# Kernel tuning notes

Hardware: AMD Instinct MI355X
Metric: run time of the kernel (lower is better)

The kernel has to match this reference:

```python
import jax, jax.numpy as jnp
import numpy as np

B, L, HIDDEN, DEPTH, INPUT_DIM = 256, 4096, 128, 2, 2
LOG_PROB_FACTOR = 0.5


def setup_inputs() -> dict:
    key = jax.random.key(0)
    k1, k2, k3, k4 = jax.random.split(key, 4)
    x = jax.random.randint(k1, (B, L), 0, INPUT_DIM)
    # variance-scaling-like init (fan_avg), small scale for recurrent stability
    W_in = jax.random.normal(k2, (INPUT_DIM, HIDDEN), dtype=jnp.float32) * np.float32(
        (2.0 / (INPUT_DIM + HIDDEN)) ** 0.5)
    W_c = jax.random.normal(k3, (DEPTH, HIDDEN, HIDDEN), dtype=jnp.float32) * np.float32(
        (0.1 / HIDDEN) ** 0.5)
    W_out = jax.random.normal(k4, (HIDDEN, INPUT_DIM - 1), dtype=jnp.float32) * np.float32(
        (2.0 / (HIDDEN + INPUT_DIM - 1)) ** 0.5)
    b_out = jnp.zeros((INPUT_DIM - 1,), dtype=jnp.float32)
    return {"x": x, "W_in": W_in, "W_c": W_c, "W_out": W_out, "b_out": b_out}


def reference(x, W_in, W_c, W_out, b_out):
    # x: [B, L] int spins; returns per-sample summed log-prob [B]
    b, l = x.shape
    input_dim = W_in.shape[0]
    depth, hidden = W_c.shape[0], W_c.shape[1]

    oh = jax.nn.one_hot(x, input_dim, dtype=W_in.dtype)       # [B, L, D_in]
    xs = jnp.moveaxis(oh, 1, 0)                                # [L, B, D_in]

    h0 = jnp.zeros((b, depth, hidden), dtype=W_in.dtype)       # zero_carry
    prev0 = jnp.zeros((b, input_dim), dtype=W_in.dtype)        # initial input

    def step(carry, x_t):
        h, prev = carry
        # data_in_dense + actFun (shared across the stack call)
        r = jax.nn.elu(prev @ W_in)                            # [B, H]
        new_h = []
        for j in range(depth):
            # RNNCell: elu(cell_carry_dense(h_j)) + input
            hj = jax.nn.elu(h[:, j] @ W_c[j]) + r              # [B, H]
            new_h.append(hj)
            r = hj
        h_new = jnp.stack(new_h, axis=1)                       # [B, depth, H]
        # output head -> normalized log-probs (realValuedOutput=True)
        logits = r @ W_out + b_out                             # [B, D_in-1]
        amp = jnp.concatenate(
            [jnp.zeros((b, 1), dtype=logits.dtype), logits], axis=-1)  # [B, D_in]
        lp = LOG_PROB_FACTOR * jax.nn.log_softmax(amp, axis=-1)
        log_p = jnp.sum(lp * x_t, axis=-1)                     # [B]
        log_p = jnp.nan_to_num(log_p, nan=-35.0)
        return (h_new, x_t), log_p

    _, log_ps = jax.lax.scan(step, (h0, prev0), xs)            # [L, B]
    return jnp.sum(log_ps, axis=0)                             # [B]
```

## Files before the change

### kernel.cpp

```cpp
#include <hip/hip_runtime.h>
#include <hip/hip_bf16.h>


#define L_LEN 4096
#define HID   128
#define NB    16
#define TPB   256
#define WPITCH 129

typedef float f32x4 __attribute__((ext_vector_type(4)));
typedef short s16x8 __attribute__((ext_vector_type(8)));
typedef short s16x4 __attribute__((ext_vector_type(4)));

__device__ __forceinline__ float eluf(float v) { return v > 0.f ? v : (__expf(v) - 1.f); }
__device__ __forceinline__ unsigned short f2bf(float v) {
    union { __hip_bfloat16 b; unsigned short u; } cv;
    cv.b = __float2bfloat16(v);
    return cv.u;
}

__global__ __launch_bounds__(TPB, 1)
void rnn_swap_kernel(const int*   __restrict__ x,
                     const float* __restrict__ W_in,
                     const float* __restrict__ W_c,
                     const float* __restrict__ W_out,
                     const float* __restrict__ b_out,
                     float* __restrict__ out)
{
    __shared__ __align__(16) unsigned short hAf[2][2][NB][HID];
    __shared__ unsigned xbsm[NB * WPITCH];
    __shared__ float gbuf[2][4][NB];

    const int T = threadIdx.x;
    const int w = T >> 6, l = T & 63, c = l & 15, g = l >> 4;
    const int bb0 = blockIdx.x * NB;
    const int swz = (c & 7) << 3;

    for (int idx = w; idx < NB * (L_LEN / 64); idx += 4) {
        int batch = idx >> 6;
        int pos   = ((idx & 63) << 6) + l;
        int v     = x[(bb0 + batch) * L_LEN + pos];
        unsigned long long mask = __ballot(v & 1);
        if (l == 0)  xbsm[batch * WPITCH + ((idx & 63) << 1)]     = (unsigned)mask;
        if (l == 32) xbsm[batch * WPITCH + ((idx & 63) << 1) + 1] = (unsigned)(mask >> 32);
    }
    for (int i = T; i < 2 * 2 * NB * HID; i += TPB) ((unsigned short*)hAf)[i] = 0;

    s16x8 Af[2][2][4];
    #pragma unroll
    for (int layer = 0; layer < 2; ++layer)
      #pragma unroll
      for (int mt = 0; mt < 2; ++mt) {
        const int col = w * 32 + mt * 16 + c;
        #pragma unroll
        for (int kt = 0; kt < 4; ++kt) {
            s16x8 f;
            #pragma unroll
            for (int j = 0; j < 8; ++j)
                f[j] = (short)f2bf(W_c[(layer * HID + kt * 32 + g * 8 + j) * HID + col]);
            Af[layer][mt][kt] = f;
        }
      }
    s16x8 woA;
    #pragma unroll
    for (int j = 0; j < 8; ++j)
        woA[j] = (c == 0) ? (short)f2bf(W_out[w * 32 + g * 8 + j]) : (short)0;

    float R0v[2][4], R1v[2][4];
    #pragma unroll
    for (int mt = 0; mt < 2; ++mt)
      #pragma unroll
      for (int r = 0; r < 4; ++r) {
        int co = w * 32 + mt * 16 + 4 * g + r;
        R0v[mt][r] = eluf(W_in[co]);
        R1v[mt][r] = eluf(W_in[HID + co]);
      }
    const float b0 = b_out[0];

    const int ro0 = (0 * 32 + g * 8) ^ swz, ro1 = (1 * 32 + g * 8) ^ swz;
    const int ro2 = (2 * 32 + g * 8) ^ swz, ro3 = (3 * 32 + g * 8) ^ swz;
    const int wo0 = (w * 32 + 0 * 16 + 4 * g) ^ swz;
    const int wo1 = (w * 32 + 1 * 16 + 4 * g) ^ swz;

    float acc = 0.f;
    unsigned xw = 0;

    __syncthreads();

#define STEP(T_, Q_) do {                                                     \
    const int t_ = (T_);                                                      \
    s16x8 B1v[4], B0v[4];                                                     \
    B1v[0] = *(const s16x8*)&hAf[Q_][1][c][ro0];                              \
    B1v[1] = *(const s16x8*)&hAf[Q_][1][c][ro1];                              \
    B1v[2] = *(const s16x8*)&hAf[Q_][1][c][ro2];                              \
    B1v[3] = *(const s16x8*)&hAf[Q_][1][c][ro3];                              \
    if (t_ < L_LEN) {                                                         \
        B0v[0] = *(const s16x8*)&hAf[Q_][0][c][ro0];                          \
        B0v[1] = *(const s16x8*)&hAf[Q_][0][c][ro1];                          \
        B0v[2] = *(const s16x8*)&hAf[Q_][0][c][ro2];                          \
        B0v[3] = *(const s16x8*)&hAf[Q_][0][c][ro3];                          \
        if (((t_ - 1) & 31) == 0) xw = xbsm[c * WPITCH + ((t_ - 1) >> 5)];    \
    }                                                                         \
    {                               \
        s16x8 Bw = (w == 0) ? B1v[0] : (w == 1) ? B1v[1]                      \
                 : (w == 2) ? B1v[2] : B1v[3];                                \
        f32x4 Cg = {0.f, 0.f, 0.f, 0.f};                                      \
        Cg = __builtin_amdgcn_mfma_f32_16x16x32_bf16(woA, Bw, Cg, 0, 0, 0);   \
        if (g == 0) gbuf[Q_][w][c] = Cg[0];                                   \
    }                                                                         \
    if (t_ > 1 && T < NB) {                         \
        int s = t_ - 2;                                                       \
        float gg = gbuf[Q_ ^ 1][0][T] + gbuf[Q_ ^ 1][1][T]                    \
                 + gbuf[Q_ ^ 1][2][T] + gbuf[Q_ ^ 1][3][T] + b0;              \
        unsigned cw = xbsm[T * WPITCH + (s >> 5)];                            \
        int bit = (cw >> (s & 31)) & 1;                                       \
        float mm  = fmaxf(gg, 0.f);                                           \
        float lse = mm + __logf(__expf(gg - mm) + __expf(-mm));               \
        acc += 0.5f * ((bit ? gg : 0.f) - lse);                               \
    }                                                                         \
    if (t_ < L_LEN) {                                                         \
        f32x4 C0v[2], C1v[2];                                                 \
        _Pragma("unroll")                                                     \
        for (int mt = 0; mt < 2; ++mt) {                                      \
            f32x4 c0 = {0.f, 0.f, 0.f, 0.f};                                  \
            f32x4 c1 = {0.f, 0.f, 0.f, 0.f};                                  \
            _Pragma("unroll")                                                 \
            for (int kt = 0; kt < 4; ++kt) {                                  \
                c0 = __builtin_amdgcn_mfma_f32_16x16x32_bf16(                 \
                        Af[0][mt][kt], B0v[kt], c0, 0, 0, 0);                 \
                c1 = __builtin_amdgcn_mfma_f32_16x16x32_bf16(                 \
                        Af[1][mt][kt], B1v[kt], c1, 0, 0, 0);                 \
            }                                                                 \
            C0v[mt] = c0; C1v[mt] = c1;                                       \
        }                                                                     \
        const int bit = (int)((xw >> ((t_ - 1) & 31)) & 1u);                  \
        _Pragma("unroll")                                                     \
        for (int mt = 0; mt < 2; ++mt) {                                      \
            s16x4 p0, p1;                                                     \
            _Pragma("unroll")                                                 \
            for (int r = 0; r < 4; ++r) {                                     \
                float h0 = eluf(C0v[mt][r]) + (bit ? R1v[mt][r] : R0v[mt][r]);\
                float h1 = eluf(C1v[mt][r]) + h0;                             \
                p0[r] = (short)f2bf(h0);                                      \
                p1[r] = (short)f2bf(h1);                                      \
            }                                                                 \
            const int wof = (mt == 0) ? wo0 : wo1;                            \
            *(s16x4*)&hAf[Q_ ^ 1][0][c][wof] = p0;                            \
            *(s16x4*)&hAf[Q_ ^ 1][1][c][wof] = p1;                            \
        }                                                                     \
    }                                                                         \
    __syncthreads();                                                          \
} while (0)

    for (int t = 1; t <= L_LEN; t += 2) {
        STEP(t, 1);
        STEP(t + 1, 0);
    }
#undef STEP

    if (T < NB) {
        float gg = gbuf[0][0][T] + gbuf[0][1][T] + gbuf[0][2][T] + gbuf[0][3][T] + b0;
        unsigned cw = xbsm[T * WPITCH + ((L_LEN - 1) >> 5)];
        int bit = (cw >> ((L_LEN - 1) & 31)) & 1;
        float mm  = fmaxf(gg, 0.f);
        float lse = mm + __logf(__expf(gg - mm) + __expf(-mm));
        acc += 0.5f * ((bit ? gg : 0.f) - lse);
        out[bb0 + T] = acc;
    }
}

extern "C" void kernel_launch(void* const* d_in, const int* in_sizes, int n_in,
                              void* d_out, int out_size, void* d_ws, size_t ws_size,
                              hipStream_t stream)
{
    const int*   x     = (const int*)  d_in[0];
    const float* W_in  = (const float*)d_in[1];
    const float* W_c   = (const float*)d_in[2];
    const float* W_out = (const float*)d_in[3];
    const float* b_out = (const float*)d_in[4];
    float* out = (float*)d_out;

    rnn_swap_kernel<<<16, TPB, 0, stream>>>(x, W_in, W_c, W_out, b_out, out);
}
```

Baseline: 3.129 ms.

## Pack two independent 16-batch groups per block with 512 threads

Each block now runs two independent 16-sample recurrences, one per 256-thread half. Shared hidden-state, gate and spin-bit buffers gain a group index, and the grid shrinks from 16 to 8 blocks. The goal is to interleave two independent dependency chains on the same compute unit to hide MFMA and LDS latency. The cost is double the work per SIMD at each step and a block-wide barrier across 8 waves instead of 4. The LDS swizzle also widens from (c&7)<<3 to c<<3, which changes the bank-conflict pattern.

```diff
diff --git a/kernel.cpp b/kernel.cpp
--- a/kernel.cpp
+++ b/kernel.cpp
@@ -4,8 +4,7 @@
 
 #define L_LEN 4096
 #define HID   128
-#define NB    16
-#define TPB   256
+#define TPB   512
 #define WPITCH 129
 
 typedef float f32x4 __attribute__((ext_vector_type(4)));
@@ -20,23 +19,27 @@
 }
 
 __global__ __launch_bounds__(TPB, 1)
-void rnn_swap_kernel(const int*   __restrict__ x,
-                     const float* __restrict__ W_in,
-                     const float* __restrict__ W_c,
-                     const float* __restrict__ W_out,
-                     const float* __restrict__ b_out,
-                     float* __restrict__ out)
+void rnn_g2_kernel(const int*   __restrict__ x,
+                   const float* __restrict__ W_in,
+                   const float* __restrict__ W_c,
+                   const float* __restrict__ W_out,
+                   const float* __restrict__ b_out,
+                   float* __restrict__ out)
 {
-    __shared__ __align__(16) unsigned short hAf[2][2][NB][HID];
-    __shared__ unsigned xbsm[NB * WPITCH];
-    __shared__ float gbuf[2][4][NB];
+    __shared__ __align__(16) unsigned short hAf[2][2][2][16][HID];
+    __shared__ unsigned xbsm[32 * WPITCH];
+    __shared__ float gbuf[2][2][4][16];
 
-    const int T = threadIdx.x;
-    const int w = T >> 6, l = T & 63, c = l & 15, g = l >> 4;
-    const int bb0 = blockIdx.x * NB;
-    const int swz = (c & 7) << 3;
+    const int T  = threadIdx.x;
+    const int w8 = T >> 6;
+    const int wg = T >> 8;
+    const int w  = w8 & 3;
+    const int l  = T & 63, c = l & 15, g = l >> 4;
+    const int grpT = T & 255;
+    const int bb0 = blockIdx.x * 32;
+    const int swz = c << 3;
 
-    for (int idx = w; idx < NB * (L_LEN / 64); idx += 4) {
+    for (int idx = w8; idx < 32 * (L_LEN / 64); idx += 8) {
         int batch = idx >> 6;
         int pos   = ((idx & 63) << 6) + l;
         int v     = x[(bb0 + batch) * L_LEN + pos];
@@ -44,7 +47,7 @@
         if (l == 0)  xbsm[batch * WPITCH + ((idx & 63) << 1)]     = (unsigned)mask;
         if (l == 32) xbsm[batch * WPITCH + ((idx & 63) << 1) + 1] = (unsigned)(mask >> 32);
     }
-    for (int i = T; i < 2 * 2 * NB * HID; i += TPB) ((unsigned short*)hAf)[i] = 0;
+    for (int i = T; i < 2 * 2 * 2 * 16 * HID; i += TPB) ((unsigned short*)hAf)[i] = 0;
 
     s16x8 Af[2][2][4];
     #pragma unroll
@@ -90,29 +93,30 @@
 #define STEP(T_, Q_) do {                                                     \
     const int t_ = (T_);                                                      \
     s16x8 B1v[4], B0v[4];                                                     \
-    B1v[0] = *(const s16x8*)&hAf[Q_][1][c][ro0];                              \
-    B1v[1] = *(const s16x8*)&hAf[Q_][1][c][ro1];                              \
-    B1v[2] = *(const s16x8*)&hAf[Q_][1][c][ro2];                              \
-    B1v[3] = *(const s16x8*)&hAf[Q_][1][c][ro3];                              \
+    B1v[0] = *(const s16x8*)&hAf[wg][Q_][1][c][ro0];                          \
+    B1v[1] = *(const s16x8*)&hAf[wg][Q_][1][c][ro1];                          \
+    B1v[2] = *(const s16x8*)&hAf[wg][Q_][1][c][ro2];                          \
+    B1v[3] = *(const s16x8*)&hAf[wg][Q_][1][c][ro3];                          \
     if (t_ < L_LEN) {                                                         \
-        B0v[0] = *(const s16x8*)&hAf[Q_][0][c][ro0];                          \
-        B0v[1] = *(const s16x8*)&hAf[Q_][0][c][ro1];                          \
-        B0v[2] = *(const s16x8*)&hAf[Q_][0][c][ro2];                          \
-        B0v[3] = *(const s16x8*)&hAf[Q_][0][c][ro3];                          \
-        if (((t_ - 1) & 31) == 0) xw = xbsm[c * WPITCH + ((t_ - 1) >> 5)];    \
+        B0v[0] = *(const s16x8*)&hAf[wg][Q_][0][c][ro0];                      \
+        B0v[1] = *(const s16x8*)&hAf[wg][Q_][0][c][ro1];                      \
+        B0v[2] = *(const s16x8*)&hAf[wg][Q_][0][c][ro2];                      \
+        B0v[3] = *(const s16x8*)&hAf[wg][Q_][0][c][ro3];                      \
+        if (((t_ - 1) & 31) == 0)                                             \
+            xw = xbsm[(wg * 16 + c) * WPITCH + ((t_ - 1) >> 5)];              \
     }                                                                         \
     {                               \
         s16x8 Bw = (w == 0) ? B1v[0] : (w == 1) ? B1v[1]                      \
                  : (w == 2) ? B1v[2] : B1v[3];                                \
         f32x4 Cg = {0.f, 0.f, 0.f, 0.f};                                      \
         Cg = __builtin_amdgcn_mfma_f32_16x16x32_bf16(woA, Bw, Cg, 0, 0, 0);   \
-        if (g == 0) gbuf[Q_][w][c] = Cg[0];                                   \
+        if (g == 0) gbuf[Q_][wg][w][c] = Cg[0];                               \
     }                                                                         \
-    if (t_ > 1 && T < NB) {                         \
+    if (t_ > 1 && grpT < 16) {                      \
         int s = t_ - 2;                                                       \
-        float gg = gbuf[Q_ ^ 1][0][T] + gbuf[Q_ ^ 1][1][T]                    \
-                 + gbuf[Q_ ^ 1][2][T] + gbuf[Q_ ^ 1][3][T] + b0;              \
-        unsigned cw = xbsm[T * WPITCH + (s >> 5)];                            \
+        float gg = gbuf[Q_ ^ 1][wg][0][grpT] + gbuf[Q_ ^ 1][wg][1][grpT]      \
+                 + gbuf[Q_ ^ 1][wg][2][grpT] + gbuf[Q_ ^ 1][wg][3][grpT] + b0;\
+        unsigned cw = xbsm[(wg * 16 + grpT) * WPITCH + (s >> 5)];             \
         int bit = (cw >> (s & 31)) & 1;                                       \
         float mm  = fmaxf(gg, 0.f);                                           \
         float lse = mm + __logf(__expf(gg - mm) + __expf(-mm));               \
@@ -145,8 +149,8 @@
                 p1[r] = (short)f2bf(h1);                                      \
             }                                                                 \
             const int wof = (mt == 0) ? wo0 : wo1;                            \
-            *(s16x4*)&hAf[Q_ ^ 1][0][c][wof] = p0;                            \
-            *(s16x4*)&hAf[Q_ ^ 1][1][c][wof] = p1;                            \
+            *(s16x4*)&hAf[wg][Q_ ^ 1][0][c][wof] = p0;                        \
+            *(s16x4*)&hAf[wg][Q_ ^ 1][1][c][wof] = p1;                        \
         }                                                                     \
     }                                                                         \
     __syncthreads();                                                          \
@@ -158,14 +162,15 @@
     }
 #undef STEP
 
-    if (T < NB) {
-        float gg = gbuf[0][0][T] + gbuf[0][1][T] + gbuf[0][2][T] + gbuf[0][3][T] + b0;
-        unsigned cw = xbsm[T * WPITCH + ((L_LEN - 1) >> 5)];
+    if (grpT < 16) {
+        float gg = gbuf[0][wg][0][grpT] + gbuf[0][wg][1][grpT]
+                 + gbuf[0][wg][2][grpT] + gbuf[0][wg][3][grpT] + b0;
+        unsigned cw = xbsm[(wg * 16 + grpT) * WPITCH + ((L_LEN - 1) >> 5)];
         int bit = (cw >> ((L_LEN - 1) & 31)) & 1;
         float mm  = fmaxf(gg, 0.f);
         float lse = mm + __logf(__expf(gg - mm) + __expf(-mm));
         acc += 0.5f * ((bit ? gg : 0.f) - lse);
-        out[bb0 + T] = acc;
+        out[bb0 + wg * 16 + grpT] = acc;
     }
 }
 
@@ -180,5 +185,5 @@
     const float* b_out = (const float*)d_in[4];
     float* out = (float*)d_out;
 
-    rnn_swap_kernel<<<16, TPB, 0, stream>>>(x, W_in, W_c, W_out, b_out, out);
+    rnn_g2_kernel<<<8, TPB, 0, stream>>>(x, W_in, W_c, W_out, b_out, out);
 }
```

Result: slower. 3.854 ms (+23.2%).

## Split the two RNN layers across separate wave groups with 512 threads

Applied to the files above, without the earlier changes.

Doubles the block to 8 waves and assigns layer 0 and layer 1 to separate groups of four waves, so each wave holds one layer's weights and issues half as many MFMAs per step. Layer 1 now needs layer 0's freshly written output, so each step adds a second barrier and a bf16 read back through LDS instead of adding in fp32 registers. The LDS swizzle also changes from (c&7)<<3 to c<<3. The aim is to shorten the per-step critical path of the serial recurrence, at the cost of an extra __syncthreads per step and extra bf16 rounding of the layer-0 state added into layer 1.

```diff
diff --git a/kernel.cpp b/kernel.cpp
--- a/kernel.cpp
+++ b/kernel.cpp
@@ -5,7 +5,7 @@
 #define L_LEN 4096
 #define HID   128
 #define NB    16
-#define TPB   256
+#define TPB   512
 #define WPITCH 129
 
 typedef float f32x4 __attribute__((ext_vector_type(4)));
@@ -18,25 +18,33 @@
     cv.b = __float2bfloat16(v);
     return cv.u;
 }
+__device__ __forceinline__ float bf2f(unsigned short u) {
+    union { float f; unsigned v; } cv;
+    cv.v = ((unsigned)u) << 16;
+    return cv.f;
+}
 
 __global__ __launch_bounds__(TPB, 1)
-void rnn_swap_kernel(const int*   __restrict__ x,
-                     const float* __restrict__ W_in,
-                     const float* __restrict__ W_c,
-                     const float* __restrict__ W_out,
-                     const float* __restrict__ b_out,
-                     float* __restrict__ out)
+void rnn_ls_kernel(const int*   __restrict__ x,
+                   const float* __restrict__ W_in,
+                   const float* __restrict__ W_c,
+                   const float* __restrict__ W_out,
+                   const float* __restrict__ b_out,
+                   float* __restrict__ out)
 {
     __shared__ __align__(16) unsigned short hAf[2][2][NB][HID];
     __shared__ unsigned xbsm[NB * WPITCH];
     __shared__ float gbuf[2][4][NB];
 
-    const int T = threadIdx.x;
-    const int w = T >> 6, l = T & 63, c = l & 15, g = l >> 4;
+    const int T  = threadIdx.x;
+    const int w8 = T >> 6;
+    const int Lw = w8 >> 2;
+    const int wv = w8 & 3;
+    const int l  = T & 63, c = l & 15, g = l >> 4;
     const int bb0 = blockIdx.x * NB;
-    const int swz = (c & 7) << 3;
+    const int swz = c << 3;
 
-    for (int idx = w; idx < NB * (L_LEN / 64); idx += 4) {
+    for (int idx = w8; idx < NB * (L_LEN / 64); idx += 8) {
         int batch = idx >> 6;
         int pos   = ((idx & 63) << 6) + l;
         int v     = x[(bb0 + batch) * L_LEN + pos];
@@ -46,110 +54,107 @@
     }
     for (int i = T; i < 2 * 2 * NB * HID; i += TPB) ((unsigned short*)hAf)[i] = 0;
 
-    s16x8 Af[2][2][4];
+    s16x8 Af[2][4];
     #pragma unroll
-    for (int layer = 0; layer < 2; ++layer)
-      #pragma unroll
-      for (int mt = 0; mt < 2; ++mt) {
-        const int col = w * 32 + mt * 16 + c;
+    for (int mt = 0; mt < 2; ++mt) {
+        const int col = wv * 32 + mt * 16 + c;
         #pragma unroll
         for (int kt = 0; kt < 4; ++kt) {
             s16x8 f;
             #pragma unroll
             for (int j = 0; j < 8; ++j)
-                f[j] = (short)f2bf(W_c[(layer * HID + kt * 32 + g * 8 + j) * HID + col]);
-            Af[layer][mt][kt] = f;
+                f[j] = (short)f2bf(W_c[(Lw * HID + kt * 32 + g * 8 + j) * HID + col]);
+            Af[mt][kt] = f;
         }
-      }
+    }
     s16x8 woA;
     #pragma unroll
     for (int j = 0; j < 8; ++j)
-        woA[j] = (c == 0) ? (short)f2bf(W_out[w * 32 + g * 8 + j]) : (short)0;
+        woA[j] = (c == 0) ? (short)f2bf(W_out[wv * 32 + g * 8 + j]) : (short)0;
 
     float R0v[2][4], R1v[2][4];
     #pragma unroll
     for (int mt = 0; mt < 2; ++mt)
       #pragma unroll
       for (int r = 0; r < 4; ++r) {
-        int co = w * 32 + mt * 16 + 4 * g + r;
+        int co = wv * 32 + mt * 16 + 4 * g + r;
         R0v[mt][r] = eluf(W_in[co]);
         R1v[mt][r] = eluf(W_in[HID + co]);
       }
     const float b0 = b_out[0];
 
-    const int ro0 = (0 * 32 + g * 8) ^ swz, ro1 = (1 * 32 + g * 8) ^ swz;
-    const int ro2 = (2 * 32 + g * 8) ^ swz, ro3 = (3 * 32 + g * 8) ^ swz;
-    const int wo0 = (w * 32 + 0 * 16 + 4 * g) ^ swz;
-    const int wo1 = (w * 32 + 1 * 16 + 4 * g) ^ swz;
+    const int ro0 = (g * 8) ^ swz,      ro1 = (32 + g * 8) ^ swz;
+    const int ro2 = (64 + g * 8) ^ swz, ro3 = (96 + g * 8) ^ swz;
+    const int wo0 = (wv * 32 + 4 * g) ^ swz;
+    const int wo1 = (wv * 32 + 16 + 4 * g) ^ swz;
 
     float acc = 0.f;
     unsigned xw = 0;
 
     __syncthreads();
 
-#define STEP(T_, Q_) do {                                                     \
-    const int t_ = (T_);                                                      \
-    s16x8 B1v[4], B0v[4];                                                     \
-    B1v[0] = *(const s16x8*)&hAf[Q_][1][c][ro0];                              \
-    B1v[1] = *(const s16x8*)&hAf[Q_][1][c][ro1];                              \
-    B1v[2] = *(const s16x8*)&hAf[Q_][1][c][ro2];                              \
-    B1v[3] = *(const s16x8*)&hAf[Q_][1][c][ro3];                              \
-    if (t_ < L_LEN) {                                                         \
-        B0v[0] = *(const s16x8*)&hAf[Q_][0][c][ro0];                          \
-        B0v[1] = *(const s16x8*)&hAf[Q_][0][c][ro1];                          \
-        B0v[2] = *(const s16x8*)&hAf[Q_][0][c][ro2];                          \
-        B0v[3] = *(const s16x8*)&hAf[Q_][0][c][ro3];                          \
-        if (((t_ - 1) & 31) == 0) xw = xbsm[c * WPITCH + ((t_ - 1) >> 5)];    \
-    }                                                                         \
-    {                               \
-        s16x8 Bw = (w == 0) ? B1v[0] : (w == 1) ? B1v[1]                      \
-                 : (w == 2) ? B1v[2] : B1v[3];                                \
-        f32x4 Cg = {0.f, 0.f, 0.f, 0.f};                                      \
-        Cg = __builtin_amdgcn_mfma_f32_16x16x32_bf16(woA, Bw, Cg, 0, 0, 0);   \
-        if (g == 0) gbuf[Q_][w][c] = Cg[0];                                   \
-    }                                                                         \
-    if (t_ > 1 && T < NB) {                         \
-        int s = t_ - 2;                                                       \
-        float gg = gbuf[Q_ ^ 1][0][T] + gbuf[Q_ ^ 1][1][T]                    \
-                 + gbuf[Q_ ^ 1][2][T] + gbuf[Q_ ^ 1][3][T] + b0;              \
-        unsigned cw = xbsm[T * WPITCH + (s >> 5)];                            \
-        int bit = (cw >> (s & 31)) & 1;                                       \
-        float mm  = fmaxf(gg, 0.f);                                           \
-        float lse = mm + __logf(__expf(gg - mm) + __expf(-mm));               \
-        acc += 0.5f * ((bit ? gg : 0.f) - lse);                               \
-    }                                                                         \
-    if (t_ < L_LEN) {                                                         \
-        f32x4 C0v[2], C1v[2];                                                 \
-        _Pragma("unroll")                                                     \
-        for (int mt = 0; mt < 2; ++mt) {                                      \
-            f32x4 c0 = {0.f, 0.f, 0.f, 0.f};                                  \
-            f32x4 c1 = {0.f, 0.f, 0.f, 0.f};                                  \
-            _Pragma("unroll")                                                 \
-            for (int kt = 0; kt < 4; ++kt) {                                  \
-                c0 = __builtin_amdgcn_mfma_f32_16x16x32_bf16(                 \
-                        Af[0][mt][kt], B0v[kt], c0, 0, 0, 0);                 \
-                c1 = __builtin_amdgcn_mfma_f32_16x16x32_bf16(                 \
-                        Af[1][mt][kt], B1v[kt], c1, 0, 0, 0);                 \
-            }                                                                 \
-            C0v[mt] = c0; C1v[mt] = c1;                                       \
-        }                                                                     \
-        const int bit = (int)((xw >> ((t_ - 1) & 31)) & 1u);                  \
-        _Pragma("unroll")                                                     \
-        for (int mt = 0; mt < 2; ++mt) {                                      \
-            s16x4 p0, p1;                                                     \
-            _Pragma("unroll")                                                 \
-            for (int r = 0; r < 4; ++r) {                                     \
-                float h0 = eluf(C0v[mt][r]) + (bit ? R1v[mt][r] : R0v[mt][r]);\
-                float h1 = eluf(C1v[mt][r]) + h0;                             \
-                p0[r] = (short)f2bf(h0);                                      \
-                p1[r] = (short)f2bf(h1);                                      \
-            }                                                                 \
-            const int wof = (mt == 0) ? wo0 : wo1;                            \
-            *(s16x4*)&hAf[Q_ ^ 1][0][c][wof] = p0;                            \
-            *(s16x4*)&hAf[Q_ ^ 1][1][c][wof] = p1;                            \
-        }                                                                     \
-    }                                                                         \
-    __syncthreads();                                                          \
+#define STEP(T_, Q_) do {                                                         \
+    const int t_ = (T_);                                                          \
+    s16x8 Bv0, Bv1, Bv2, Bv3;                                                     \
+    if ((Lw == 1) || (t_ < L_LEN)) {                                              \
+        Bv0 = *(const s16x8*)&hAf[Q_][Lw][c][ro0];                                \
+        Bv1 = *(const s16x8*)&hAf[Q_][Lw][c][ro1];                                \
+        Bv2 = *(const s16x8*)&hAf[Q_][Lw][c][ro2];                                \
+        Bv3 = *(const s16x8*)&hAf[Q_][Lw][c][ro3];                                \
+    }                                                                             \
+    if (Lw == 1) {                   \
+        s16x8 Bw = (wv == 0) ? Bv0 : (wv == 1) ? Bv1 : (wv == 2) ? Bv2 : Bv3;     \
+        f32x4 Cg = {0.f, 0.f, 0.f, 0.f};                                          \
+        Cg = __builtin_amdgcn_mfma_f32_16x16x32_bf16(woA, Bw, Cg, 0, 0, 0);       \
+        if (g == 0) gbuf[Q_][wv][c] = Cg[0];                                      \
+    }                                                                             \
+    if (w8 == 7 && l < 16 && t_ > 1) {                \
+        int s_ = t_ - 2;                                                          \
+        float gg = gbuf[Q_ ^ 1][0][c] + gbuf[Q_ ^ 1][1][c]                        \
+                 + gbuf[Q_ ^ 1][2][c] + gbuf[Q_ ^ 1][3][c] + b0;                  \
+        unsigned cw = xbsm[c * WPITCH + (s_ >> 5)];                               \
+        int bit = (cw >> (s_ & 31)) & 1;                                          \
+        float mm  = fmaxf(gg, 0.f);                                               \
+        float lse = mm + __logf(__expf(gg - mm) + __expf(-mm));                   \
+        acc += 0.5f * ((bit ? gg : 0.f) - lse);                                   \
+    }                                                                             \
+    f32x4 CA = {0.f, 0.f, 0.f, 0.f}, CB = {0.f, 0.f, 0.f, 0.f};                   \
+    if (t_ < L_LEN) {                                                             \
+        CA = __builtin_amdgcn_mfma_f32_16x16x32_bf16(Af[0][0], Bv0, CA, 0, 0, 0); \
+        CA = __builtin_amdgcn_mfma_f32_16x16x32_bf16(Af[0][1], Bv1, CA, 0, 0, 0); \
+        CA = __builtin_amdgcn_mfma_f32_16x16x32_bf16(Af[0][2], Bv2, CA, 0, 0, 0); \
+        CA = __builtin_amdgcn_mfma_f32_16x16x32_bf16(Af[0][3], Bv3, CA, 0, 0, 0); \
+        CB = __builtin_amdgcn_mfma_f32_16x16x32_bf16(Af[1][0], Bv0, CB, 0, 0, 0); \
+        CB = __builtin_amdgcn_mfma_f32_16x16x32_bf16(Af[1][1], Bv1, CB, 0, 0, 0); \
+        CB = __builtin_amdgcn_mfma_f32_16x16x32_bf16(Af[1][2], Bv2, CB, 0, 0, 0); \
+        CB = __builtin_amdgcn_mfma_f32_16x16x32_bf16(Af[1][3], Bv3, CB, 0, 0, 0); \
+        if (Lw == 0) {                   \
+            if (((t_ - 1) & 31) == 0) xw = xbsm[c * WPITCH + ((t_ - 1) >> 5)];    \
+            const int bit = (int)((xw >> ((t_ - 1) & 31)) & 1u);                  \
+            s16x4 p0, p1;                                                         \
+            _Pragma("unroll")                                                     \
+            for (int r = 0; r < 4; ++r) {                                         \
+                p0[r] = (short)f2bf(eluf(CA[r]) + (bit ? R1v[0][r] : R0v[0][r])); \
+                p1[r] = (short)f2bf(eluf(CB[r]) + (bit ? R1v[1][r] : R0v[1][r])); \
+            }                                                                     \
+            *(s16x4*)&hAf[Q_ ^ 1][0][c][wo0] = p0;                                \
+            *(s16x4*)&hAf[Q_ ^ 1][0][c][wo1] = p1;                                \
+        }                                                                         \
+    }                                                                             \
+    __syncthreads();                                                              \
+    if (Lw == 1 && t_ < L_LEN) {            \
+        s16x4 h0a = *(const s16x4*)&hAf[Q_ ^ 1][0][c][wo0];                       \
+        s16x4 h0b = *(const s16x4*)&hAf[Q_ ^ 1][0][c][wo1];                       \
+        s16x4 p0, p1;                                                             \
+        _Pragma("unroll")                                                         \
+        for (int r = 0; r < 4; ++r) {                                             \
+            p0[r] = (short)f2bf(eluf(CA[r]) + bf2f((unsigned short)h0a[r]));      \
+            p1[r] = (short)f2bf(eluf(CB[r]) + bf2f((unsigned short)h0b[r]));      \
+        }                                                                         \
+        *(s16x4*)&hAf[Q_ ^ 1][1][c][wo0] = p0;                                    \
+        *(s16x4*)&hAf[Q_ ^ 1][1][c][wo1] = p1;                                    \
+    }                                                                             \
+    __syncthreads();                                                              \
 } while (0)
 
     for (int t = 1; t <= L_LEN; t += 2) {
@@ -158,14 +163,14 @@
     }
 #undef STEP
 
-    if (T < NB) {
-        float gg = gbuf[0][0][T] + gbuf[0][1][T] + gbuf[0][2][T] + gbuf[0][3][T] + b0;
-        unsigned cw = xbsm[T * WPITCH + ((L_LEN - 1) >> 5)];
+    if (w8 == 7 && l < 16) {
+        float gg = gbuf[0][0][c] + gbuf[0][1][c] + gbuf[0][2][c] + gbuf[0][3][c] + b0;
+        unsigned cw = xbsm[c * WPITCH + ((L_LEN - 1) >> 5)];
         int bit = (cw >> ((L_LEN - 1) & 31)) & 1;
         float mm  = fmaxf(gg, 0.f);
         float lse = mm + __logf(__expf(gg - mm) + __expf(-mm));
         acc += 0.5f * ((bit ? gg : 0.f) - lse);
-        out[bb0 + T] = acc;
+        out[bb0 + c] = acc;
     }
 }
 
@@ -180,5 +185,5 @@
     const float* b_out = (const float*)d_in[4];
     float* out = (float*)d_out;
 
-    rnn_swap_kernel<<<16, TPB, 0, stream>>>(x, W_in, W_c, W_out, b_out, out);
+    rnn_ls_kernel<<<16, TPB, 0, stream>>>(x, W_in, W_c, W_out, b_out, out);
 }
```

Result: faster. 2.756 ms (-11.9%).
